# Kernel optimization log

Measured on AMD Instinct MI355X. Metric: run time of the kernel, lower is better.

The kernel has to match this reference:

```python
import jax, jax.numpy as jnp
import numpy as np

EPS = 1e-5
NPOINT = 1024
NSAMPLE = 32


def _bn(x, gamma, beta, axes):
    # batch-norm in training mode (biased variance), channel-last
    m = jnp.mean(x, axes, keepdims=True)
    v = jnp.var(x, axes, keepdims=True)
    return (x - m) * jax.lax.rsqrt(v + EPS) * gamma + beta


def _fps(xyz, npoint):
    # xyz: [B, N, 3] -> indices [B, npoint]; deterministic start at index 0
    xyz = jax.lax.stop_gradient(xyz)
    B, N, _ = xyz.shape

    def step(carry, _):
        dist, far = carry
        c = jnp.take_along_axis(xyz, far[:, None, None], axis=1)  # [B,1,3]
        d = jnp.sum((xyz - c) ** 2, -1)                            # [B,N]
        dist = jnp.minimum(dist, d)
        return (dist, jnp.argmax(dist, -1).astype(jnp.int32)), far

    init = (jnp.full((B, N), 1e10, xyz.dtype), jnp.zeros((B,), jnp.int32))
    _, idx = jax.lax.scan(step, init, None, length=npoint)
    return idx.T  # [B, npoint]


def _sqdist(src, dst):
    # [B,S,C],[B,N,C] -> [B,S,N]
    d = -2.0 * jnp.einsum('bsc,bnc->bsn', src, dst)
    d += jnp.sum(src ** 2, -1)[:, :, None]
    d += jnp.sum(dst ** 2, -1)[:, None, :]
    return d


def _gather(p, idx):
    # p: [B,N,C], idx: [B,...] -> [B,...,C]
    return jax.vmap(lambda a, i: a[i])(p, idx)


def setup_inputs() -> dict:
    key = jax.random.key(0)
    ks = jax.random.split(key, 12)
    B, N, D = 8, 4096, 64
    inp = {
        'xyz': jax.random.normal(ks[0], (B, 3, N), jnp.float32),
        'points': jax.random.normal(ks[1], (B, D, N), jnp.float32),
        # mlp convs (1x1 Conv2d == per-point linear): [out,in]
        'c1_w': jax.random.normal(ks[2], (64, 64), jnp.float32) / 8.0,
        'c1_b': jnp.zeros((64,), jnp.float32),
        'g1': jnp.ones((64,), jnp.float32), 'b1': jnp.zeros((64,), jnp.float32),
        'c2_w': jax.random.normal(ks[3], (128, 64), jnp.float32) / 8.0,
        'c2_b': jnp.zeros((128,), jnp.float32),
        'g2': jnp.ones((128,), jnp.float32), 'b2': jnp.zeros((128,), jnp.float32),
        # weightnet: 3 -> 8 -> 8 -> 16
        'w0_w': jax.random.normal(ks[4], (8, 3), jnp.float32) / np.sqrt(3.0),
        'w0_b': jnp.zeros((8,), jnp.float32),
        'w0_g': jnp.ones((8,), jnp.float32), 'w0_be': jnp.zeros((8,), jnp.float32),
        'w1_w': jax.random.normal(ks[5], (8, 8), jnp.float32) / np.sqrt(8.0),
        'w1_b': jnp.zeros((8,), jnp.float32),
        'w1_g': jnp.ones((8,), jnp.float32), 'w1_be': jnp.zeros((8,), jnp.float32),
        'w2_w': jax.random.normal(ks[6], (16, 8), jnp.float32) / np.sqrt(8.0),
        'w2_b': jnp.zeros((16,), jnp.float32),
        'w2_g': jnp.ones((16,), jnp.float32), 'w2_be': jnp.zeros((16,), jnp.float32),
        # final linear: 16*128 -> 128
        'lin_w': jax.random.normal(ks[7], (128, 16 * 128), jnp.float32) / np.sqrt(2048.0),
        'lin_b': jnp.zeros((128,), jnp.float32),
        'lg': jnp.ones((128,), jnp.float32), 'lb': jnp.zeros((128,), jnp.float32),
    }
    return inp


def reference(xyz, points, c1_w, c1_b, g1, b1, c2_w, c2_b, g2, b2,
              w0_w, w0_b, w0_g, w0_be, w1_w, w1_b, w1_g, w1_be,
              w2_w, w2_b, w2_g, w2_be, lin_w, lin_b, lg, lb):
    B = xyz.shape[0]
    X = jnp.transpose(xyz, (0, 2, 1))      # [B,N,3]
    P = jnp.transpose(points, (0, 2, 1))   # [B,N,D]

    fps_idx = _fps(X, NPOINT)                                      # [B,S]
    new_xyz = jnp.take_along_axis(X, fps_idx[:, :, None], axis=1)  # [B,S,3]

    sqr = _sqdist(jax.lax.stop_gradient(new_xyz), jax.lax.stop_gradient(X))
    _, nidx = jax.lax.top_k(-sqr, NSAMPLE)                         # [B,S,K]

    neigh_xyz = _gather(X, nidx)                                   # [B,S,K,3]
    off = neigh_xyz - new_xyz[:, :, None, :]                       # [B,S,K,3]
    f = _gather(P, nidx)                                           # [B,S,K,D]

    # per-point MLP (1x1 convs + BN2d over (B,K,S) + relu)
    for W, bias, g, be in ((c1_w, c1_b, g1, b1), (c2_w, c2_b, g2, b2)):
        f = jax.nn.relu(_bn(jnp.einsum('bskd,cd->bskc', f, W) + bias, g, be, (0, 1, 2)))

    # WeightNet on offsets
    w = off
    for W, bias, g, be in ((w0_w, w0_b, w0_g, w0_be),
                           (w1_w, w1_b, w1_g, w1_be),
                           (w2_w, w2_b, w2_g, w2_be)):
        w = jax.nn.relu(_bn(jnp.einsum('bskd,cd->bskc', w, W) + bias, g, be, (0, 1, 2)))

    # weighted aggregation over neighbors: [B,S,Cl,16] -> [B,S,Cl*16]
    feats = jnp.einsum('bskc,bskw->bscw', f, w).reshape(B, NPOINT, -1)
    y = feats @ lin_w.T + lin_b                                    # [B,S,128]
    y = jax.nn.relu(_bn(y, lg, lb, (0, 1)))

    return jnp.transpose(new_xyz, (0, 2, 1)), jnp.transpose(y, (0, 2, 1))
```

## Files before the change

kernel.cpp:

```cpp
#include <hip/hip_runtime.h>
#include <hip/hip_bf16.h>

#define BB 8
#define NN 4096
#define DD 64
#define SS 1024
#define KK 32
#define C1 64
#define C2 128

typedef unsigned int uint32;
typedef unsigned long long uint64;

constexpr int BSK = BB * SS * KK;
constexpr int BS  = BB * SS;

#define ST_S1_C1 0
#define ST_S2_C1 64
#define ST_S1_C2 128
#define ST_S2_C2 256
#define ST_S1_W0 384
#define ST_S2_W0 392
#define ST_S1_W1 400
#define ST_S2_W1 408
#define ST_S1_W2 416
#define ST_S2_W2 432
#define ST_S1_Y  448
#define ST_S2_Y  576
#define ST_STRIDE 704
#define N_SLOTS 64

#define PA_A_C1 0
#define PA_C_C1 64
#define PA_A_C2 128
#define PA_C_C2 256
#define PA_A_W0 384
#define PA_C_W0 392
#define PA_A_W1 400
#define PA_C_W1 408
#define PA_A_W2 416
#define PA_C_W2 432
#define PA_A_Y  448
#define PA_C_Y  576

#if __has_builtin(__builtin_amdgcn_update_dpp)
#define HAS_DPP 1
template <int CTRL>
__device__ __forceinline__ double dpp_f64(double x) {
    uint64 u = (uint64)__double_as_longlong(x);
    int lo = (int)(uint32)u, hi = (int)(uint32)(u >> 32);
    int lo2 = __builtin_amdgcn_update_dpp(lo, lo, CTRL, 0xf, 0xf, false);
    int hi2 = __builtin_amdgcn_update_dpp(hi, hi, CTRL, 0xf, 0xf, false);
    return __longlong_as_double((long long)(((uint64)(uint32)hi2 << 32) | (uint32)lo2));
}
__device__ __forceinline__ double wave_max_pack(double k) {
    k = fmax(k, dpp_f64<0x111>(k));
    k = fmax(k, dpp_f64<0x112>(k));
    k = fmax(k, dpp_f64<0x114>(k));
    k = fmax(k, dpp_f64<0x118>(k));
    k = fmax(k, dpp_f64<0x142>(k));
    k = fmax(k, dpp_f64<0x143>(k));
    return k;
}
__device__ __forceinline__ double wave_min_pack(double k) {
    k = fmin(k, dpp_f64<0x111>(k));
    k = fmin(k, dpp_f64<0x112>(k));
    k = fmin(k, dpp_f64<0x114>(k));
    k = fmin(k, dpp_f64<0x118>(k));
    k = fmin(k, dpp_f64<0x142>(k));
    k = fmin(k, dpp_f64<0x143>(k));
    return k;
}
__device__ __forceinline__ uint64 bcast63_u64(double k) {
#if __has_builtin(__builtin_amdgcn_readlane)
    uint64 u = (uint64)__double_as_longlong(k);
    int lo = __builtin_amdgcn_readlane((int)(uint32)u, 63);
    int hi = __builtin_amdgcn_readlane((int)(uint32)(u >> 32), 63);
    return ((uint64)(uint32)hi << 32) | (uint32)lo;
#else
    return (uint64)__double_as_longlong(__shfl(k, 63));
#endif
}
#define FPS_WRITER_LANE 63
template <int CTRL>
__device__ __forceinline__ float dpp_mov_f32(float x) {
    int r = __builtin_amdgcn_update_dpp(__float_as_int(x), __float_as_int(x),
                                        CTRL, 0xf, 0xf, false);
    return __int_as_float(r);
}
__device__ __forceinline__ float wave_sum_f32(float v) {
    v += dpp_mov_f32<0x111>(v);
    v += dpp_mov_f32<0x112>(v);
    v += dpp_mov_f32<0x114>(v);
    v += dpp_mov_f32<0x118>(v);
    v += dpp_mov_f32<0x142>(v);
    v += dpp_mov_f32<0x143>(v);
    return v;
}
#define LIN_WRITER 63
#else
#define HAS_DPP 0
__device__ __forceinline__ double wave_max_pack(double k) {
#pragma unroll
    for (int m = 32; m >= 1; m >>= 1) k = fmax(k, __shfl_xor(k, m));
    return k;
}
__device__ __forceinline__ double wave_min_pack(double k) {
#pragma unroll
    for (int m = 32; m >= 1; m >>= 1) k = fmin(k, __shfl_xor(k, m));
    return k;
}
__device__ __forceinline__ uint64 bcast63_u64(double k) {
    return (uint64)__double_as_longlong(k);
}
#define FPS_WRITER_LANE 0
__device__ __forceinline__ float wave_sum_f32(float v) {
#pragma unroll
    for (int m = 32; m >= 1; m >>= 1) v += __shfl_xor(v, m);
    return v;
}
#define LIN_WRITER 0
#endif

__device__ __forceinline__ uint32 bf16rne(float x) {
    uint32 u = __float_as_uint(x);
    return (u + 0x7fffu + ((u >> 16) & 1u)) >> 16;
}

typedef __attribute__((ext_vector_type(8))) short bf16x8;
typedef __attribute__((ext_vector_type(4))) float f32x4v;

__global__ __launch_bounds__(256) void prep_fps(const float* __restrict__ points,
                                                __hip_bfloat16* __restrict__ ptsT,
                                                const float* __restrict__ c1_w,
                                                const float* __restrict__ c2_w,
                                                const float* __restrict__ lin_w,
                                                float* __restrict__ w1t,
                                                float* __restrict__ w2t,
                                                __hip_bfloat16* __restrict__ linB,
                                                const float* __restrict__ xyz,
                                                float* __restrict__ new_xyz,
                                                float* __restrict__ out0) {
    __shared__ __align__(16) char smu[69696];
    int t = threadIdx.x;
    int blk = blockIdx.x;
    if (blk < 8) {
        float4* xyz4 = (float4*)smu;
        int* hist = (int*)(smu + 65536);
        double* slots = (double*)(smu + 69632);
        int b = blk;
        int wv = t >> 6, lane = t & 63;
        const float* base = xyz + (size_t)b * 3 * NN;
        float px[16], py[16], pz[16], dl[16];
        uint32 lidx[16];
#pragma unroll
        for (int i = 0; i < 16; i++) {
            int n = t + 256 * i;
            px[i] = base[n];
            py[i] = base[NN + n];
            pz[i] = base[2 * NN + n];
            float4 v; v.x = px[i]; v.y = py[i]; v.z = pz[i]; v.w = 0.f;
            xyz4[n] = v;
            dl[i] = 1e10f;
            lidx[i] = (uint32)(NN - 1 - n);
        }
        if (t == 0) hist[0] = 0;
        __syncthreads();
        int far = 0;
        for (int step = 1; step < SS; step++) {
            int p = step & 1;
            float4 c = xyz4[far];
            float cx = c.x, cy = c.y, cz = c.z;
            double k0 = 0.0, k1 = 0.0, k2 = 0.0, k3 = 0.0;
#pragma unroll
            for (int i = 0; i < 16; i++) {
                float dx = __fsub_rn(px[i], cx);
                float dy = __fsub_rn(py[i], cy);
                float dz = __fsub_rn(pz[i], cz);
                float d = __fadd_rn(__fadd_rn(__fmul_rn(dx, dx), __fmul_rn(dy, dy)),
                                    __fmul_rn(dz, dz));
                float nd = fminf(dl[i], d);
                dl[i] = nd;
                uint64 kbits = ((uint64)__float_as_uint(nd) << 32) | lidx[i];
                double kk = __longlong_as_double((long long)kbits);
                if ((i & 3) == 0) k0 = fmax(k0, kk);
                else if ((i & 3) == 1) k1 = fmax(k1, kk);
                else if ((i & 3) == 2) k2 = fmax(k2, kk);
                else k3 = fmax(k3, kk);
            }
            double kbest = fmax(fmax(k0, k1), fmax(k2, k3));
            kbest = wave_max_pack(kbest);
            if (lane == FPS_WRITER_LANE) slots[p * 4 + wv] = kbest;
            __syncthreads();
            double s0 = slots[p * 4 + 0], s1 = slots[p * 4 + 1];
            double s2 = slots[p * 4 + 2], s3 = slots[p * 4 + 3];
            double bk = fmax(fmax(s0, s1), fmax(s2, s3));
            uint64 kb = (uint64)__double_as_longlong(bk);
            int bbx = (NN - 1) - (int)(uint32)(kb & 0xffffffffull);
            far = bbx;
            if (t == 0) hist[step] = bbx;
        }
        __syncthreads();
        for (int s = t; s < SS; s += 256) {
            int idx = hist[s];
            float4 v = xyz4[idx];
            size_t q = (size_t)(b * SS + s);
            new_xyz[q * 3 + 0] = v.x;
            new_xyz[q * 3 + 1] = v.y;
            new_xyz[q * 3 + 2] = v.z;
            out0[(size_t)b * 3 * SS + 0 * SS + s] = v.x;
            out0[(size_t)b * 3 * SS + 1 * SS + s] = v.y;
            out0[(size_t)b * 3 * SS + 2 * SS + s] = v.z;
        }
    } else if (blk < 520) {
        float (*tile)[65] = (float(*)[65])smu;
        int bb = blk - 8;
        int b = bb >> 6;
        int n0 = (bb & 63) * 64;
        for (int i = t; i < 4096; i += 256) {
            int d = i >> 6, n = i & 63;
            tile[d][n] = points[((size_t)b * DD + d) * NN + n0 + n];
        }
        __syncthreads();
        for (int i = t; i < 4096; i += 256) {
            int n = i >> 6, d = i & 63;
            ptsT[((size_t)b * NN + n0 + n) * DD + d] = __float2bfloat16(tile[d][n]);
        }
    } else {
        int i = (blk - 520) * 256 + t;
        if (i < 4096) {
            int d = i >> 6, c = i & 63;
            w1t[d * 64 + c] = c1_w[c * 64 + d];
        }
        int j = i - 4096;
        if (j >= 0 && j < 8192) {
            int d = j >> 7, c = j & 127;
            w2t[d * 128 + c] = c2_w[c * 64 + d];
        }
        int l = i - 12288;
        if (l >= 0 && l < 262144) linB[l] = __float2bfloat16(lin_w[l]);
    }
}

__global__ __launch_bounds__(256) void knn_wave(const float* __restrict__ xyz,
                                                const float* __restrict__ new_xyz,
                                                int* __restrict__ nidx,
                                                float* __restrict__ offs) {
    int wv = threadIdx.x >> 6, lane = threadIdx.x & 63;
    int q = blockIdx.x * 4 + wv;
    int b = q >> 10;
    const float* base = xyz + (size_t)b * 3 * NN;
    float sx = new_xyz[(size_t)q * 3 + 0];
    float sy = new_xyz[(size_t)q * 3 + 1];
    float sz = new_xyz[(size_t)q * 3 + 2];
    float s2 = __fadd_rn(__fadd_rn(__fmul_rn(sx, sx), __fmul_rn(sy, sy)), __fmul_rn(sz, sz));
    float dl[64];
#pragma unroll
    for (int i = 0; i < 64; i++) {
        int n = i * 64 + lane;
        float x = base[n], y = base[NN + n], z = base[2 * NN + n];
        float d2 = __fadd_rn(__fadd_rn(__fmul_rn(x, x), __fmul_rn(y, y)), __fmul_rn(z, z));
        float dot = __fadd_rn(__fadd_rn(__fmul_rn(sx, x), __fmul_rn(sy, y)), __fmul_rn(sz, z));
        float v = __fmul_rn(-2.0f, dot);
        v = __fadd_rn(v, s2);
        v = __fadd_rn(v, d2);
        dl[i] = v;
    }
    const float MASKF = __uint_as_float(0x7F7FFFFFu);
    unsigned long long excl = 0ull;
    for (int k = 0; k < KK; k++) {
        float best = MASKF;
        int bslot = 0;
#pragma unroll
        for (int i = 0; i < 64; i++) {
            bool ok = ((excl >> i) & 1ull) == 0ull;
            float v = ok ? dl[i] : MASKF;
            if (v < best) { best = v; bslot = i; }
        }
        uint64 kbits = ((uint64)__float_as_uint(best) << 32) |
                       (uint32)(bslot * 64 + lane);
        double kb = wave_min_pack(__longlong_as_double((long long)kbits));
        uint64 r = bcast63_u64(kb);
        int bi = (int)(uint32)(r & 0xffffffffull);
        if ((bi & 63) == lane) excl |= (1ull << (bi >> 6));
        if (lane == 0) {
            nidx[(size_t)q * KK + k] = bi;
            size_t oo = ((size_t)q * KK + k) * 3;
            offs[oo + 0] = __fsub_rn(base[bi], sx);
            offs[oo + 1] = __fsub_rn(base[NN + bi], sy);
            offs[oo + 2] = __fsub_rn(base[2 * NN + bi], sz);
        }
    }
}

__device__ __forceinline__ void stage_pts(const __hip_bfloat16* __restrict__ ptsT,
                                          const int* __restrict__ nidx,
                                          int q, int b, int t, float* pts) {
    int k = t >> 3, d8 = t & 7;
    int nn = nidx[(size_t)q * KK + k];
    uint4 u = ((const uint4*)ptsT)[((size_t)b * NN + nn) * 8 + d8];
    float4 lo, hi;
    lo.x = __uint_as_float(u.x << 16); lo.y = __uint_as_float(u.x & 0xffff0000u);
    lo.z = __uint_as_float(u.y << 16); lo.w = __uint_as_float(u.y & 0xffff0000u);
    hi.x = __uint_as_float(u.z << 16); hi.y = __uint_as_float(u.z & 0xffff0000u);
    hi.z = __uint_as_float(u.w << 16); hi.w = __uint_as_float(u.w & 0xffff0000u);
    *(float4*)&pts[k * 64 + d8 * 8] = lo;
    *(float4*)&pts[k * 64 + d8 * 8 + 4] = hi;
}

__global__ __launch_bounds__(256) void pass_a(const __hip_bfloat16* __restrict__ ptsT,
                                              const int* __restrict__ nidx,
                                              const float* __restrict__ offs,
                                              const float* __restrict__ w1t,
                                              const float* __restrict__ c1_b,
                                              const float* __restrict__ w0_w,
                                              const float* __restrict__ w0_b,
                                              float* __restrict__ stats,
                                              float* __restrict__ f1pre,
                                              int emit_f1) {
    __shared__ __align__(16) float pts[2048];
    __shared__ float red1[256], red2[256];
    int blk = blockIdx.x, t = threadIdx.x;
    int b = blk >> 10;
    int slot = blk & (N_SLOTS - 1);
    stage_pts(ptsT, nidx, blk, b, t, pts);
    __syncthreads();
    int c = t & 63, kg = t >> 6;
    float bias = c1_b[c];
    float acc[8];
#pragma unroll
    for (int j = 0; j < 8; j++) acc[j] = bias;
    for (int d4 = 0; d4 < 16; d4++) {
        float w0 = w1t[(4 * d4 + 0) * 64 + c];
        float w1v = w1t[(4 * d4 + 1) * 64 + c];
        float w2v = w1t[(4 * d4 + 2) * 64 + c];
        float w3 = w1t[(4 * d4 + 3) * 64 + c];
#pragma unroll
        for (int j = 0; j < 8; j++) {
            const float4 p = *(const float4*)&pts[(kg + 4 * j) * 64 + 4 * d4];
            acc[j] = fmaf(p.x, w0, acc[j]);
            acc[j] = fmaf(p.y, w1v, acc[j]);
            acc[j] = fmaf(p.z, w2v, acc[j]);
            acc[j] = fmaf(p.w, w3, acc[j]);
        }
    }
    if (emit_f1) {
#pragma unroll
        for (int j = 0; j < 8; j++)
            f1pre[(size_t)blk * 2048 + j * 256 + t] = acc[j];
    }
    float s1 = 0.f, s2 = 0.f;
#pragma unroll
    for (int j = 0; j < 8; j++) { s1 += acc[j]; s2 += acc[j] * acc[j]; }
    red1[t] = s1;
    red2[t] = s2;
    __syncthreads();
    if (t < 64) {
        atomicAdd(&stats[slot * ST_STRIDE + ST_S1_C1 + t],
                  red1[t] + red1[t + 64] + red1[t + 128] + red1[t + 192]);
        atomicAdd(&stats[slot * ST_STRIDE + ST_S2_C1 + t],
                  red2[t] + red2[t + 64] + red2[t + 128] + red2[t + 192]);
    }
    int k0 = t >> 3, c0 = t & 7;
    size_t oo = ((size_t)blk * KK + k0) * 3;
    float h = w0_b[c0];
    h = fmaf(offs[oo + 0], w0_w[c0 * 3 + 0], h);
    h = fmaf(offs[oo + 1], w0_w[c0 * 3 + 1], h);
    h = fmaf(offs[oo + 2], w0_w[c0 * 3 + 2], h);
    __syncthreads();
    red1[t] = h;
    red2[t] = h * h;
    __syncthreads();
    if (t < 8) {
        float a = 0.f, q = 0.f;
        for (int j = t; j < 256; j += 8) { a += red1[j]; q += red2[j]; }
        atomicAdd(&stats[slot * ST_STRIDE + ST_S1_W0 + t], a);
        atomicAdd(&stats[slot * ST_STRIDE + ST_S2_W0 + t], q);
    }
}

__device__ __forceinline__ void fin_one(const float* stats, float* params,
                                        const float* g, const float* be,
                                        int s1o, int s2o, int ao, int co,
                                        int nch, float inv, int t) {
    if (t < nch) {
        float s1 = 0.f, s2 = 0.f;
        for (int s = 0; s < N_SLOTS; s++) {
            s1 += stats[s * ST_STRIDE + s1o + t];
            s2 += stats[s * ST_STRIDE + s2o + t];
        }
        float m = s1 * inv;
        float v = s2 * inv - m * m;
        float a = g[t] * rsqrtf(v + 1e-5f);
        params[ao + t] = a;
        params[co + t] = be[t] - m * a;
    }
}

__global__ void finalize_bn(const float* __restrict__ stats, float* __restrict__ params,
                            const float* __restrict__ g, const float* __restrict__ be,
                            int s1o, int s2o, int ao, int co, int nch, float inv) {
    fin_one(stats, params, g, be, s1o, s2o, ao, co, nch, inv, threadIdx.x);
}

__global__ void finalize_two(const float* __restrict__ stats, float* __restrict__ params,
                             const float* __restrict__ gA, const float* __restrict__ beA,
                             int s1A, int s2A, int aA, int cA, int nA, float invA,
                             const float* __restrict__ gB, const float* __restrict__ beB,
                             int s1B, int s2B, int aB, int cB, int nB, float invB) {
    if (blockIdx.x == 0)
        fin_one(stats, params, gA, beA, s1A, s2A, aA, cA, nA, invA, threadIdx.x);
    else
        fin_one(stats, params, gB, beB, s1B, s2B, aB, cB, nB, invB, threadIdx.x);
}

__global__ __launch_bounds__(256) void pass_b(const __hip_bfloat16* __restrict__ ptsT,
                                              const int* __restrict__ nidx,
                                              const float* __restrict__ offs,
                                              const float* __restrict__ w1t,
                                              const float* __restrict__ c1_b,
                                              const float* __restrict__ w2t,
                                              const float* __restrict__ c2_b,
                                              const float* __restrict__ w0_w,
                                              const float* __restrict__ w0_b,
                                              const float* __restrict__ w1_w,
                                              const float* __restrict__ w1_b,
                                              const float* __restrict__ params,
                                              float* __restrict__ stats) {
    __shared__ __align__(16) float pts[2048];
    __shared__ __align__(16) float f1[2048];
    __shared__ float red1[256], red2[256];
    int blk = blockIdx.x, t = threadIdx.x;
    int b = blk >> 10;
    int slot = blk & (N_SLOTS - 1);
    stage_pts(ptsT, nidx, blk, b, t, pts);
    __syncthreads();
    {
        int c = t & 63, kg = t >> 6;
        float a1 = params[PA_A_C1 + c], cc1 = params[PA_C_C1 + c], bias = c1_b[c];
        float acc[8];
#pragma unroll
        for (int j = 0; j < 8; j++) acc[j] = bias;
        for (int d4 = 0; d4 < 16; d4++) {
// ... 239 lines not shown
#pragma unroll
        for (int q = 0; q < 8; q++) h = fmaf(h1[q], w2_w[cw * 8 + q], h);
        wg[idx] = fmaxf(fmaf(h, params[PA_A_W2 + cw], params[PA_C_W2 + cw]), 0.f);
    }
}

__global__ __launch_bounds__(256) void tail_nl2(const float* __restrict__ f2pre,
                                                const float* __restrict__ offs,
                                                const float* __restrict__ w0_w,
                                                const float* __restrict__ w0_b,
                                                const float* __restrict__ w1_w,
                                                const float* __restrict__ w1_b,
                                                const float* __restrict__ w2_w,
                                                const float* __restrict__ w2_b,
                                                const float* __restrict__ params,
                                                float* __restrict__ featsF) {
    __shared__ __align__(16) float sm[6656];
    float* f2    = sm;
    float* wg    = sm + 4096;
    float* feats = sm + 4608;
    int blk = blockIdx.x, t = threadIdx.x;
    weightnet_to_lds(offs, w0_w, w0_b, w1_w, w1_b, w2_w, w2_b, params, blk, t, wg);
    {
        int c = t & 127;
        float a2 = params[PA_A_C2 + c], cc2 = params[PA_C_C2 + c];
#pragma unroll
        for (int i = 0; i < 16; i++) {
            float v = f2pre[(size_t)blk * 4096 + i * 256 + t];
            f2[i * 256 + t] = fmaxf(fmaf(v, a2, cc2), 0.f);
        }
    }
    __syncthreads();
    {
        int cc = t & 127, wh = t >> 7;
        float acc[8];
#pragma unroll
        for (int i = 0; i < 8; i++) acc[i] = 0.f;
        for (int k = 0; k < KK; k++) {
            float fv = f2[k * 128 + cc];
            const float4 wa = *(const float4*)&wg[k * 16 + 8 * wh];
            const float4 wb = *(const float4*)&wg[k * 16 + 8 * wh + 4];
            acc[0] = fmaf(fv, wa.x, acc[0]);
            acc[1] = fmaf(fv, wa.y, acc[1]);
            acc[2] = fmaf(fv, wa.z, acc[2]);
            acc[3] = fmaf(fv, wa.w, acc[3]);
            acc[4] = fmaf(fv, wb.x, acc[4]);
            acc[5] = fmaf(fv, wb.y, acc[5]);
            acc[6] = fmaf(fv, wb.z, acc[6]);
            acc[7] = fmaf(fv, wb.w, acc[7]);
        }
        *(float4*)&feats[cc * 16 + 8 * wh]     = *(float4*)&acc[0];
        *(float4*)&feats[cc * 16 + 8 * wh + 4] = *(float4*)&acc[4];
    }
    __syncthreads();
#pragma unroll
    for (int i = 0; i < 8; i++)
        featsF[(size_t)blk * 2048 + i * 256 + t] = feats[i * 256 + t];
}

__global__ __launch_bounds__(256) void fused_tail_nl(
        const __hip_bfloat16* __restrict__ ptsT, const int* __restrict__ nidx,
        const float* __restrict__ offs,
        const float* __restrict__ w1t, const float* __restrict__ c1_b,
        const float* __restrict__ w2t, const float* __restrict__ c2_b,
        const float* __restrict__ w0_w, const float* __restrict__ w0_b,
        const float* __restrict__ w1_w, const float* __restrict__ w1_b,
        const float* __restrict__ w2_w, const float* __restrict__ w2_b,
        const float* __restrict__ params, float* __restrict__ featsF) {
    __shared__ __align__(16) float sm[8704];
    float* pts   = sm;
    float* f1    = sm + 2048;
    float* f2    = sm + 4096;
    float* wg    = sm + 8192;
    int blk = blockIdx.x, t = threadIdx.x;
    int b = blk >> 10;
    stage_pts(ptsT, nidx, blk, b, t, pts);
    weightnet_to_lds(offs, w0_w, w0_b, w1_w, w1_b, w2_w, w2_b, params, blk, t, wg);
    __syncthreads();
    {
        int c = t & 63, kg = t >> 6;
        float a1 = params[PA_A_C1 + c], cc1 = params[PA_C_C1 + c], bias = c1_b[c];
        float acc[8];
#pragma unroll
        for (int j = 0; j < 8; j++) acc[j] = bias;
        for (int d4 = 0; d4 < 16; d4++) {
            float w0 = w1t[(4 * d4 + 0) * 64 + c];
            float w1v = w1t[(4 * d4 + 1) * 64 + c];
            float w2v = w1t[(4 * d4 + 2) * 64 + c];
            float w3 = w1t[(4 * d4 + 3) * 64 + c];
#pragma unroll
            for (int j = 0; j < 8; j++) {
                const float4 p = *(const float4*)&pts[(kg + 4 * j) * 64 + 4 * d4];
                acc[j] = fmaf(p.x, w0, acc[j]);
                acc[j] = fmaf(p.y, w1v, acc[j]);
                acc[j] = fmaf(p.z, w2v, acc[j]);
                acc[j] = fmaf(p.w, w3, acc[j]);
            }
        }
#pragma unroll
        for (int j = 0; j < 8; j++)
            f1[(kg + 4 * j) * 64 + c] = fmaxf(fmaf(acc[j], a1, cc1), 0.f);
    }
    __syncthreads();
    {
        int c = t & 127, kg = t >> 7;
        float a2 = params[PA_A_C2 + c], cc2 = params[PA_C_C2 + c], bias = c2_b[c];
        float acc[16];
#pragma unroll
        for (int j = 0; j < 16; j++) acc[j] = bias;
        for (int d4 = 0; d4 < 16; d4++) {
            float w0 = w2t[(4 * d4 + 0) * 128 + c];
            float w1v = w2t[(4 * d4 + 1) * 128 + c];
            float w2v = w2t[(4 * d4 + 2) * 128 + c];
            float w3 = w2t[(4 * d4 + 3) * 128 + c];
#pragma unroll
            for (int j = 0; j < 16; j++) {
                const float4 p = *(const float4*)&f1[(kg + 2 * j) * 64 + 4 * d4];
                acc[j] = fmaf(p.x, w0, acc[j]);
                acc[j] = fmaf(p.y, w1v, acc[j]);
                acc[j] = fmaf(p.z, w2v, acc[j]);
                acc[j] = fmaf(p.w, w3, acc[j]);
            }
        }
#pragma unroll
        for (int j = 0; j < 16; j++)
            f2[(kg + 2 * j) * 128 + c] = fmaxf(fmaf(acc[j], a2, cc2), 0.f);
    }
    __syncthreads();
    {
        int cc = t & 127, wh = t >> 7;
        float acc[8];
#pragma unroll
        for (int i = 0; i < 8; i++) acc[i] = 0.f;
        for (int k = 0; k < KK; k++) {
            float fv = f2[k * 128 + cc];
            const float4 wa = *(const float4*)&wg[k * 16 + 8 * wh];
            const float4 wb = *(const float4*)&wg[k * 16 + 8 * wh + 4];
            acc[0] = fmaf(fv, wa.x, acc[0]);
            acc[1] = fmaf(fv, wa.y, acc[1]);
            acc[2] = fmaf(fv, wa.z, acc[2]);
            acc[3] = fmaf(fv, wa.w, acc[3]);
            acc[4] = fmaf(fv, wb.x, acc[4]);
            acc[5] = fmaf(fv, wb.y, acc[5]);
            acc[6] = fmaf(fv, wb.z, acc[6]);
            acc[7] = fmaf(fv, wb.w, acc[7]);
        }
        *(float4*)&pts[cc * 16 + 8 * wh]     = *(float4*)&acc[0];
        *(float4*)&pts[cc * 16 + 8 * wh + 4] = *(float4*)&acc[4];
    }
    __syncthreads();
#pragma unroll
    for (int i = 0; i < 8; i++)
        featsF[(size_t)blk * 2048 + i * 256 + t] = sm[i * 256 + t];
}

__global__ __launch_bounds__(256) void fused_tail(
        const __hip_bfloat16* __restrict__ ptsT, const int* __restrict__ nidx,
        const float* __restrict__ offs,
        const float* __restrict__ w1t, const float* __restrict__ c1_b,
        const float* __restrict__ w2t, const float* __restrict__ c2_b,
        const float* __restrict__ w0_w, const float* __restrict__ w0_b,
        const float* __restrict__ w1_w, const float* __restrict__ w1_b,
        const float* __restrict__ w2_w, const float* __restrict__ w2_b,
        const __hip_bfloat16* __restrict__ linB, const float* __restrict__ lin_b,
        const float* __restrict__ params, float* __restrict__ stats,
        float* __restrict__ ypre) {
    __shared__ __align__(16) float sm[8704];
    float* pts   = sm;
    float* f1    = sm + 2048;
    float* f2    = sm + 4096;
    float* wg    = sm + 8192;
    int blk = blockIdx.x, t = threadIdx.x;
    int b = blk >> 10;
    int slot = blk & (N_SLOTS - 1);
    stage_pts(ptsT, nidx, blk, b, t, pts);
    weightnet_to_lds(offs, w0_w, w0_b, w1_w, w1_b, w2_w, w2_b, params, blk, t, wg);
    __syncthreads();
    {
        int c = t & 63, kg = t >> 6;
        float a1 = params[PA_A_C1 + c], cc1 = params[PA_C_C1 + c], bias = c1_b[c];
        float acc[8];
#pragma unroll
        for (int j = 0; j < 8; j++) acc[j] = bias;
        for (int d4 = 0; d4 < 16; d4++) {
            float w0 = w1t[(4 * d4 + 0) * 64 + c];
            float w1v = w1t[(4 * d4 + 1) * 64 + c];
            float w2v = w1t[(4 * d4 + 2) * 64 + c];
            float w3 = w1t[(4 * d4 + 3) * 64 + c];
#pragma unroll
            for (int j = 0; j < 8; j++) {
                const float4 p = *(const float4*)&pts[(kg + 4 * j) * 64 + 4 * d4];
                acc[j] = fmaf(p.x, w0, acc[j]);
                acc[j] = fmaf(p.y, w1v, acc[j]);
                acc[j] = fmaf(p.z, w2v, acc[j]);
                acc[j] = fmaf(p.w, w3, acc[j]);
            }
        }
#pragma unroll
        for (int j = 0; j < 8; j++)
            f1[(kg + 4 * j) * 64 + c] = fmaxf(fmaf(acc[j], a1, cc1), 0.f);
    }
    __syncthreads();
    {
        int c = t & 127, kg = t >> 7;
        float a2 = params[PA_A_C2 + c], cc2 = params[PA_C_C2 + c], bias = c2_b[c];
        float acc[16];
#pragma unroll
        for (int j = 0; j < 16; j++) acc[j] = bias;
        for (int d4 = 0; d4 < 16; d4++) {
            float w0 = w2t[(4 * d4 + 0) * 128 + c];
            float w1v = w2t[(4 * d4 + 1) * 128 + c];
            float w2v = w2t[(4 * d4 + 2) * 128 + c];
            float w3 = w2t[(4 * d4 + 3) * 128 + c];
#pragma unroll
            for (int j = 0; j < 16; j++) {
                const float4 p = *(const float4*)&f1[(kg + 2 * j) * 64 + 4 * d4];
                acc[j] = fmaf(p.x, w0, acc[j]);
                acc[j] = fmaf(p.y, w1v, acc[j]);
                acc[j] = fmaf(p.z, w2v, acc[j]);
                acc[j] = fmaf(p.w, w3, acc[j]);
            }
        }
#pragma unroll
        for (int j = 0; j < 16; j++)
            f2[(kg + 2 * j) * 128 + c] = fmaxf(fmaf(acc[j], a2, cc2), 0.f);
    }
    __syncthreads();
    {
        int cc = t & 127, wh = t >> 7;
        float acc[8];
#pragma unroll
        for (int i = 0; i < 8; i++) acc[i] = 0.f;
        for (int k = 0; k < KK; k++) {
            float fv = f2[k * 128 + cc];
            const float4 wa = *(const float4*)&wg[k * 16 + 8 * wh];
            const float4 wb = *(const float4*)&wg[k * 16 + 8 * wh + 4];
            acc[0] = fmaf(fv, wa.x, acc[0]);
            acc[1] = fmaf(fv, wa.y, acc[1]);
            acc[2] = fmaf(fv, wa.z, acc[2]);
            acc[3] = fmaf(fv, wa.w, acc[3]);
            acc[4] = fmaf(fv, wb.x, acc[4]);
            acc[5] = fmaf(fv, wb.y, acc[5]);
            acc[6] = fmaf(fv, wb.z, acc[6]);
            acc[7] = fmaf(fv, wb.w, acc[7]);
        }
        *(float4*)&pts[cc * 16 + 8 * wh]     = *(float4*)&acc[0];
        *(float4*)&pts[cc * 16 + 8 * wh + 4] = *(float4*)&acc[4];
    }
    __syncthreads();
    float* feats = pts;
    {
        int wv = t >> 6, lane = t & 63;
        float4 fv[8];
#pragma unroll
        for (int j0 = 0; j0 < 8; j0++)
            fv[j0] = *(const float4*)&feats[(j0 * 64 + lane) * 4];
        for (int oi = 0; oi < 32; oi++) {
            int o = wv * 32 + oi;
            const uint2* lw = (const uint2*)(linB + (size_t)o * 2048);
            float acc = 0.f;
#pragma unroll
            for (int j0 = 0; j0 < 8; j0++) {
                uint2 u = lw[j0 * 64 + lane];
                acc = fmaf(fv[j0].x, __uint_as_float(u.x << 16), acc);
                acc = fmaf(fv[j0].y, __uint_as_float(u.x & 0xffff0000u), acc);
                acc = fmaf(fv[j0].z, __uint_as_float(u.y << 16), acc);
                acc = fmaf(fv[j0].w, __uint_as_float(u.y & 0xffff0000u), acc);
            }
            acc = wave_sum_f32(acc);
            if (lane == LIN_WRITER) {
                float y = acc + lin_b[o];
                ypre[(size_t)blk * 128 + o] = y;
                atomicAdd(&stats[slot * ST_STRIDE + ST_S1_Y + o], y);
                atomicAdd(&stats[slot * ST_STRIDE + ST_S2_Y + o], y * y);
            }
        }
    }
}

__global__ __launch_bounds__(256) void linear_mm16(const float* __restrict__ featsF,
                                                   const __hip_bfloat16* __restrict__ linB,
                                                   const float* __restrict__ lin_b,
                                                   float* __restrict__ stats,
                                                   float* __restrict__ ypre) {
    __shared__ __align__(16) unsigned short Ah[2][16 * 72];
    __shared__ __align__(16) unsigned short Al[2][16 * 72];
    __shared__ __align__(16) unsigned short Bsm[2][128 * 72];
    int t = threadIdx.x;
    int q0 = blockIdx.x * 16;
    int slot = blockIdx.x & (N_SLOTS - 1);
    int qa = t >> 4, pa = t & 15;
    int ob = t >> 1, pb = t & 1;
    int lane = t & 63, w = t >> 6;
    int lg = lane >> 4, ln = lane & 15;
    int qb_base = q0 + lg * 4;

    f32x4v acc0 = {0.f, 0.f, 0.f, 0.f};
    f32x4v acc1 = {0.f, 0.f, 0.f, 0.f};

    const uint4* gA0 = (const uint4*)(featsF + (size_t)(q0 + qa) * 2048);
    const uint4* gB0 = (const uint4*)(linB + (size_t)ob * 2048);

    uint4 ra, rb0, rb1, rb2, rb3;
    ra  = gA0[pa];
    rb0 = gB0[pb * 4 + 0];
    rb1 = gB0[pb * 4 + 1];
    rb2 = gB0[pb * 4 + 2];
    rb3 = gB0[pb * 4 + 3];

    for (int kc = 0; kc < 32; kc++) {
        int buf = kc & 1;
        {
            float f0 = __uint_as_float(ra.x), f1v = __uint_as_float(ra.y);
            float f2v = __uint_as_float(ra.z), f3 = __uint_as_float(ra.w);
            uint32 h0 = bf16rne(f0), h1 = bf16rne(f1v), h2 = bf16rne(f2v), h3 = bf16rne(f3);
            uint2 hv;
            hv.x = h0 | (h1 << 16); hv.y = h2 | (h3 << 16);
            *(uint2*)&Ah[buf][qa * 72 + pa * 4] = hv;
            uint32 l0 = bf16rne(f0 - __uint_as_float(h0 << 16));
            uint32 l1 = bf16rne(f1v - __uint_as_float(h1 << 16));
            uint32 l2 = bf16rne(f2v - __uint_as_float(h2 << 16));
            uint32 l3 = bf16rne(f3 - __uint_as_float(h3 << 16));
            uint2 lv;
            lv.x = l0 | (l1 << 16); lv.y = l2 | (l3 << 16);
            *(uint2*)&Al[buf][qa * 72 + pa * 4] = lv;
            *(uint4*)&Bsm[buf][ob * 72 + pb * 32 + 0]  = rb0;
            *(uint4*)&Bsm[buf][ob * 72 + pb * 32 + 8]  = rb1;
            *(uint4*)&Bsm[buf][ob * 72 + pb * 32 + 16] = rb2;
            *(uint4*)&Bsm[buf][ob * 72 + pb * 32 + 24] = rb3;
        }
        __syncthreads();
        if (kc + 1 < 32) {
            ra  = gA0[(kc + 1) * 16 + pa];
            rb0 = gB0[(kc + 1) * 8 + pb * 4 + 0];
            rb1 = gB0[(kc + 1) * 8 + pb * 4 + 1];
            rb2 = gB0[(kc + 1) * 8 + pb * 4 + 2];
            rb3 = gB0[(kc + 1) * 8 + pb * 4 + 3];
        }
#pragma unroll
        for (int s = 0; s < 2; s++) {
            int ko = s * 32 + lg * 8;
            bf16x8 ah = *(const bf16x8*)&Ah[buf][ln * 72 + ko];
            bf16x8 al = *(const bf16x8*)&Al[buf][ln * 72 + ko];
            bf16x8 b0 = *(const bf16x8*)&Bsm[buf][(w * 32 + 0  + ln) * 72 + ko];
            bf16x8 b1 = *(const bf16x8*)&Bsm[buf][(w * 32 + 16 + ln) * 72 + ko];
            acc0 = __builtin_amdgcn_mfma_f32_16x16x32_bf16(ah, b0, acc0, 0, 0, 0);
            acc0 = __builtin_amdgcn_mfma_f32_16x16x32_bf16(al, b0, acc0, 0, 0, 0);
            acc1 = __builtin_amdgcn_mfma_f32_16x16x32_bf16(ah, b1, acc1, 0, 0, 0);
            acc1 = __builtin_amdgcn_mfma_f32_16x16x32_bf16(al, b1, acc1, 0, 0, 0);
        }
    }
    {
        int o0 = w * 32 + 0  + ln;
        int o1 = w * 32 + 16 + ln;
        float lb0 = lin_b[o0], lb1 = lin_b[o1];
        float s1a = 0.f, s2a = 0.f, s1b = 0.f, s2b = 0.f;
#pragma unroll
        for (int r = 0; r < 4; r++) {
            size_t qrow = (size_t)(qb_base + r) * 128;
            float y0 = acc0[r] + lb0;
            float y1 = acc1[r] + lb1;
            ypre[qrow + o0] = y0;
            ypre[qrow + o1] = y1;
            s1a += y0; s2a += y0 * y0;
            s1b += y1; s2b += y1 * y1;
        }
        atomicAdd(&stats[slot * ST_STRIDE + ST_S1_Y + o0], s1a);
        atomicAdd(&stats[slot * ST_STRIDE + ST_S2_Y + o0], s2a);
        atomicAdd(&stats[slot * ST_STRIDE + ST_S1_Y + o1], s1b);
        atomicAdd(&stats[slot * ST_STRIDE + ST_S2_Y + o1], s2b);
    }
}

__global__ __launch_bounds__(256) void bn_y(const float* __restrict__ ypre,
                                            const float* __restrict__ stats,
                                            const float* __restrict__ lg,
                                            const float* __restrict__ lb,
                                            float* __restrict__ out1) {
    __shared__ float tile[64 * 133];
    __shared__ float pa[128], pc[128];
    int blk = blockIdx.x;
    int b = blk >> 4;
    int s0 = (blk & 15) * 64;
    int t = threadIdx.x;
    if (t < 128) {
        float s1 = 0.f, s2 = 0.f;
        for (int s = 0; s < N_SLOTS; s++) {
            s1 += stats[s * ST_STRIDE + ST_S1_Y + t];
            s2 += stats[s * ST_STRIDE + ST_S2_Y + t];
        }
        const float inv = 1.f / (float)BS;
        float m = s1 * inv;
        float v = s2 * inv - m * m;
        float a = lg[t] * rsqrtf(v + 1e-5f);
        pa[t] = a;
        pc[t] = lb[t] - m * a;
    }
#pragma unroll
    for (int i = 0; i < 32; i++) {
        int idx = i * 256 + t;
        int s = idx >> 7, c = idx & 127;
        tile[s * 133 + c] = ypre[(((size_t)b << 10) + s0 + s) * 128 + c];
    }
    __syncthreads();
#pragma unroll
    for (int i = 0; i < 32; i++) {
        int idx = i * 256 + t;
        int c = idx >> 6, s = idx & 63;
        float v = tile[s * 133 + c];
        out1[((size_t)b * 128 + c) * 1024 + s0 + s] =
            fmaxf(fmaf(v, pa[c], pc[c]), 0.f);
    }
}

extern "C" void kernel_launch(void* const* d_in, const int* in_sizes, int n_in,
                              void* d_out, int out_size, void* d_ws, size_t ws_size,
                              hipStream_t stream) {
    const float* xyz    = (const float*)d_in[0];
    const float* points = (const float*)d_in[1];
    const float* c1_w = (const float*)d_in[2];
    const float* c1_b = (const float*)d_in[3];
    const float* g1   = (const float*)d_in[4];
    const float* b1   = (const float*)d_in[5];
    const float* c2_w = (const float*)d_in[6];
    const float* c2_b = (const float*)d_in[7];
    const float* g2   = (const float*)d_in[8];
    const float* b2   = (const float*)d_in[9];
    const float* w0_w = (const float*)d_in[10];
    const float* w0_b = (const float*)d_in[11];
    const float* w0_g = (const float*)d_in[12];
    const float* w0_be= (const float*)d_in[13];
    const float* w1_w = (const float*)d_in[14];
    const float* w1_b = (const float*)d_in[15];
    const float* w1_g = (const float*)d_in[16];
    const float* w1_be= (const float*)d_in[17];
    const float* w2_w = (const float*)d_in[18];
    const float* w2_b = (const float*)d_in[19];
    const float* w2_g = (const float*)d_in[20];
    const float* w2_be= (const float*)d_in[21];
    const float* lin_w= (const float*)d_in[22];
    const float* lin_b= (const float*)d_in[23];
    const float* lg   = (const float*)d_in[24];
    const float* lb   = (const float*)d_in[25];

    float* out0 = (float*)d_out;
    float* out1 = out0 + (size_t)BB * 3 * SS;

    char* wsb = (char*)d_ws;
    int*   nidx    = (int*)(wsb + 0);
    float* offs    = (float*)(wsb + 1048576);
    float* new_xyz = (float*)(wsb + 4194304);
    float* ypre    = (float*)(wsb + 4292608);
    __hip_bfloat16* ptsT = (__hip_bfloat16*)(wsb + 8486912);
    float* w1t     = (float*)(wsb + 12681216);
    float* w2t     = (float*)(wsb + 12697600);
    __hip_bfloat16* linB = (__hip_bfloat16*)(wsb + 12730368);
    float* stats   = (float*)(wsb + 13254656);
    float* params  = (float*)(wsb + 13434880);
    float* featsF  = (float*)(wsb + 13437696);
    float* f1pre   = featsF;
    float* f2pre   = (float*)(wsb + 80546560);

    const size_t NEED1 = 13437696ull + 67108864ull;
    const size_t NEED2 = 80546560ull + 134217728ull;
    const int tier = (ws_size >= NEED2) ? 2 : (ws_size >= NEED1) ? 1 : 0;

    hipMemsetAsync(stats, 0, N_SLOTS * ST_STRIDE * sizeof(float), stream);

    prep_fps<<<1592, 256, 0, stream>>>(points, ptsT, c1_w, c2_w, lin_w, w1t, w2t,
                                       linB, xyz, new_xyz, out0);
    knn_wave<<<BS / 4, 256, 0, stream>>>(xyz, new_xyz, nidx, offs);

    pass_a<<<BS, 256, 0, stream>>>(ptsT, nidx, offs, w1t, c1_b, w0_w, w0_b, stats,
                                   f1pre, tier == 2 ? 1 : 0);
    finalize_two<<<2, 128, 0, stream>>>(stats, params,
                                        g1, b1, ST_S1_C1, ST_S2_C1, PA_A_C1, PA_C_C1, 64, 1.f / BSK,
                                        w0_g, w0_be, ST_S1_W0, ST_S2_W0, PA_A_W0, PA_C_W0, 8, 1.f / BSK);

    if (tier == 2) {
        pass_b2<<<BS, 256, 0, stream>>>(f1pre, offs, w2t, c2_b,
                                        w0_w, w0_b, w1_w, w1_b, params, stats, f2pre);
    } else {
        pass_b<<<BS, 256, 0, stream>>>(ptsT, nidx, offs, w1t, c1_b, w2t, c2_b,
                                       w0_w, w0_b, w1_w, w1_b, params, stats);
    }
    finalize_two<<<2, 128, 0, stream>>>(stats, params,
                                        g2, b2, ST_S1_C2, ST_S2_C2, PA_A_C2, PA_C_C2, 128, 1.f / BSK,
                                        w1_g, w1_be, ST_S1_W1, ST_S2_W1, PA_A_W1, PA_C_W1, 8, 1.f / BSK);

    pass_w2<<<BSK / 256, 256, 0, stream>>>(offs, w0_w, w0_b, w1_w, w1_b, w2_w, w2_b,
                                           params, stats);
    finalize_bn<<<1, 128, 0, stream>>>(stats, params, w2_g, w2_be,
                                       ST_S1_W2, ST_S2_W2, PA_A_W2, PA_C_W2, 16, 1.f / BSK);

    if (tier == 2) {
        tail_nl2<<<BS, 256, 0, stream>>>(f2pre, offs, w0_w, w0_b, w1_w, w1_b,
                                         w2_w, w2_b, params, featsF);
        linear_mm16<<<BS / 16, 256, 0, stream>>>(featsF, linB, lin_b, stats, ypre);
    } else if (tier == 1) {
        fused_tail_nl<<<BS, 256, 0, stream>>>(ptsT, nidx, offs, w1t, c1_b, w2t, c2_b,
                                              w0_w, w0_b, w1_w, w1_b, w2_w, w2_b,
                                              params, featsF);
        linear_mm16<<<BS / 16, 256, 0, stream>>>(featsF, linB, lin_b, stats, ypre);
    } else {
        fused_tail<<<BS, 256, 0, stream>>>(ptsT, nidx, offs, w1t, c1_b, w2t, c2_b,
                                           w0_w, w0_b, w1_w, w1_b, w2_w, w2_b,
                                           linB, lin_b, params, stats, ypre);
    }

    bn_y<<<BB * 16, 256, 0, stream>>>(ypre, stats, lg, lb, out1);
}
```

Baseline: 1.113 ms.

## Fuse FPS and kNN into one kernel with progress-flag streaming

Merges the FPS/prep kernel and the kNN kernel into a single launch. FPS blocks publish new_xyz in chunks of 32 sampled points and advance a per-batch progress counter with release atomics, while kNN blocks spin with acquire loads until the centroids they need exist. kNN work then overlaps the long serial FPS loop instead of waiting for it to finish. This risks deadlock if kNN blocks occupy all CUs before the FPS blocks are scheduled, adds spin-wait overhead, and removes the tier-0 fused_tail fallback.

Result: no change. 1.109 ms (-0.3%).

```diff
diff --git a/kernel.cpp b/kernel.cpp
--- a/kernel.cpp
+++ b/kernel.cpp
@@ -40,8 +40,6 @@
 #define PA_C_W1 408
 #define PA_A_W2 416
 #define PA_C_W2 432
-#define PA_A_Y  448
-#define PA_C_Y  576
 
 #if __has_builtin(__builtin_amdgcn_update_dpp)
 #define HAS_DPP 1
@@ -130,17 +128,20 @@
 typedef __attribute__((ext_vector_type(8))) short bf16x8;
 typedef __attribute__((ext_vector_type(4))) float f32x4v;
 
-__global__ __launch_bounds__(256) void prep_fps(const float* __restrict__ points,
-                                                __hip_bfloat16* __restrict__ ptsT,
-                                                const float* __restrict__ c1_w,
-                                                const float* __restrict__ c2_w,
-                                                const float* __restrict__ lin_w,
-                                                float* __restrict__ w1t,
-                                                float* __restrict__ w2t,
-                                                __hip_bfloat16* __restrict__ linB,
-                                                const float* __restrict__ xyz,
-                                                float* __restrict__ new_xyz,
-                                                float* __restrict__ out0) {
+__global__ __launch_bounds__(256) void prep_fps_knn(const float* __restrict__ points,
+                                                    __hip_bfloat16* __restrict__ ptsT,
+                                                    const float* __restrict__ c1_w,
+                                                    const float* __restrict__ c2_w,
+                                                    const float* __restrict__ lin_w,
+                                                    float* __restrict__ w1t,
+                                                    float* __restrict__ w2t,
+                                                    __hip_bfloat16* __restrict__ linB,
+                                                    const float* __restrict__ xyz,
+                                                    float* __restrict__ new_xyz,
+                                                    float* __restrict__ out0,
+                                                    int* __restrict__ progress,
+                                                    int* __restrict__ nidx,
+                                                    float* __restrict__ offs) {
     __shared__ __align__(16) char smu[69696];
     int t = threadIdx.x;
     int blk = blockIdx.x;
@@ -199,6 +200,20 @@
             int bbx = (NN - 1) - (int)(uint32)(kb & 0xffffffffull);
             far = bbx;
             if (t == 0) hist[step] = bbx;
+            if ((step & 31) == 1 && step > 32) {
+                if (t < 32) {
+                    int s2p = step - 33 + t;
+                    int idx2 = hist[s2p];
+                    float4 v2 = xyz4[idx2];
+                    size_t qq = (size_t)(b * SS + s2p) * 3;
+                    new_xyz[qq + 0] = v2.x;
+                    new_xyz[qq + 1] = v2.y;
+                    new_xyz[qq + 2] = v2.z;
+                }
+                if (t == 0)
+                    __hip_atomic_store(&progress[b], step - 1, __ATOMIC_RELEASE,
+                                       __HIP_MEMORY_SCOPE_AGENT);
+            }
         }
         __syncthreads();
         for (int s = t; s < SS; s += 256) {
@@ -212,6 +227,11 @@
             out0[(size_t)b * 3 * SS + 1 * SS + s] = v.y;
             out0[(size_t)b * 3 * SS + 2 * SS + s] = v.z;
         }
+        __threadfence();
+        __syncthreads();
+        if (t == 0)
+            __hip_atomic_store(&progress[b], SS, __ATOMIC_RELEASE,
+                               __HIP_MEMORY_SCOPE_AGENT);
     } else if (blk < 520) {
         float (*tile)[65] = (float(*)[65])smu;
         int bb = blk - 8;
@@ -226,7 +246,7 @@
             int n = i >> 6, d = i & 63;
             ptsT[((size_t)b * NN + n0 + n) * DD + d] = __float2bfloat16(tile[d][n]);
         }
-    } else {
+    } else if (blk < 1592) {
         int i = (blk - 520) * 256 + t;
         if (i < 4096) {
             int d = i >> 6, c = i & 63;
@@ -239,56 +259,57 @@
         }
         int l = i - 12288;
         if (l >= 0 && l < 262144) linB[l] = __float2bfloat16(lin_w[l]);
-    }
-}
-
-__global__ __launch_bounds__(256) void knn_wave(const float* __restrict__ xyz,
-                                                const float* __restrict__ new_xyz,
-                                                int* __restrict__ nidx,
-                                                float* __restrict__ offs) {
-    int wv = threadIdx.x >> 6, lane = threadIdx.x & 63;
-    int q = blockIdx.x * 4 + wv;
-    int b = q >> 10;
-    const float* base = xyz + (size_t)b * 3 * NN;
-    float sx = new_xyz[(size_t)q * 3 + 0];
-    float sy = new_xyz[(size_t)q * 3 + 1];
-    float sz = new_xyz[(size_t)q * 3 + 2];
-    float s2 = __fadd_rn(__fadd_rn(__fmul_rn(sx, sx), __fmul_rn(sy, sy)), __fmul_rn(sz, sz));
-    float dl[64];
-#pragma unroll
-    for (int i = 0; i < 64; i++) {
-        int n = i * 64 + lane;
-        float x = base[n], y = base[NN + n], z = base[2 * NN + n];
-        float d2 = __fadd_rn(__fadd_rn(__fmul_rn(x, x), __fmul_rn(y, y)), __fmul_rn(z, z));
-        float dot = __fadd_rn(__fadd_rn(__fmul_rn(sx, x), __fmul_rn(sy, y)), __fmul_rn(sz, z));
-        float v = __fmul_rn(-2.0f, dot);
-        v = __fadd_rn(v, s2);
-        v = __fadd_rn(v, d2);
-        dl[i] = v;
-    }
-    const float MASKF = __uint_as_float(0x7F7FFFFFu);
-    unsigned long long excl = 0ull;
-    for (int k = 0; k < KK; k++) {
-        float best = MASKF;
-        int bslot = 0;
+    } else {
+        int cb = blk - 1592;
+        int wv = t >> 6, lane = t & 63;
+        int bq = cb & 7;
+        int pos = ((cb >> 3) << 2) + wv;
+        int q = bq * SS + pos;
+        int needed = pos + 1;
+        while (__hip_atomic_load(&progress[bq], __ATOMIC_ACQUIRE,
+                                 __HIP_MEMORY_SCOPE_AGENT) < needed)
+            __builtin_amdgcn_s_sleep(8);
+        const float* base = xyz + (size_t)bq * 3 * NN;
+        float sx = new_xyz[(size_t)q * 3 + 0];
+        float sy = new_xyz[(size_t)q * 3 + 1];
+        float sz = new_xyz[(size_t)q * 3 + 2];
+        float s2 = __fadd_rn(__fadd_rn(__fmul_rn(sx, sx), __fmul_rn(sy, sy)), __fmul_rn(sz, sz));
+        float dl[64];
 #pragma unroll
         for (int i = 0; i < 64; i++) {
-            bool ok = ((excl >> i) & 1ull) == 0ull;
-            float v = ok ? dl[i] : MASKF;
-            if (v < best) { best = v; bslot = i; }
-        }
-        uint64 kbits = ((uint64)__float_as_uint(best) << 32) |
-                       (uint32)(bslot * 64 + lane);
-        double kb = wave_min_pack(__longlong_as_double((long long)kbits));
-        uint64 r = bcast63_u64(kb);
-        int bi = (int)(uint32)(r & 0xffffffffull);
-        if ((bi & 63) == lane) excl |= (1ull << (bi >> 6));
-        if (lane == 0) {
-            nidx[(size_t)q * KK + k] = bi;
-            size_t oo = ((size_t)q * KK + k) * 3;
-            offs[oo + 0] = __fsub_rn(base[bi], sx);
-            offs[oo + 1] = __fsub_rn(base[NN + bi], sy);
-            offs[oo + 2] = __fsub_rn(base[2 * NN + bi], sz);
+            int n = i * 64 + lane;
+            float x = base[n], y = base[NN + n], z = base[2 * NN + n];
+            float d2 = __fadd_rn(__fadd_rn(__fmul_rn(x, x), __fmul_rn(y, y)), __fmul_rn(z, z));
+            float dot = __fadd_rn(__fadd_rn(__fmul_rn(sx, x), __fmul_rn(sy, y)), __fmul_rn(sz, z));
+            float v = __fmul_rn(-2.0f, dot);
+            v = __fadd_rn(v, s2);
+            v = __fadd_rn(v, d2);
+            dl[i] = v;
+        }
+        const float MASKF = __uint_as_float(0x7F7FFFFFu);
+        unsigned long long excl = 0ull;
+        for (int k = 0; k < KK; k++) {
+            float best = MASKF;
+            int bslot = 0;
+#pragma unroll
+            for (int i = 0; i < 64; i++) {
+                bool ok = ((excl >> i) & 1ull) == 0ull;
+                float v = ok ? dl[i] : MASKF;
+                if (v < best) { best = v; bslot = i; }
+            }
+            uint64 kbits = ((uint64)__float_as_uint(best) << 32) |
+                           (uint32)(bslot * 64 + lane);
+            double kb = wave_min_pack(__longlong_as_double((long long)kbits));
+            uint64 r = bcast63_u64(kb);
+            int bi = (int)(uint32)(r & 0xffffffffull);
+            if ((bi & 63) == lane) excl |= (1ull << (bi >> 6));
+            if (lane == 0) {
+                nidx[(size_t)q * KK + k] = bi;
+                size_t oo = ((size_t)q * KK + k) * 3;
+                offs[oo + 0] = __fsub_rn(base[bi], sx);
+                offs[oo + 1] = __fsub_rn(base[NN + bi], sy);
+                offs[oo + 2] = __fsub_rn(base[2 * NN + bi], sz);
+            }
         }
     }
 }
@@ -834,130 +855,6 @@
 #pragma unroll
     for (int i = 0; i < 8; i++)
         featsF[(size_t)blk * 2048 + i * 256 + t] = sm[i * 256 + t];
-}
-
-__global__ __launch_bounds__(256) void fused_tail(
-        const __hip_bfloat16* __restrict__ ptsT, const int* __restrict__ nidx,
-        const float* __restrict__ offs,
-        const float* __restrict__ w1t, const float* __restrict__ c1_b,
-        const float* __restrict__ w2t, const float* __restrict__ c2_b,
-        const float* __restrict__ w0_w, const float* __restrict__ w0_b,
-        const float* __restrict__ w1_w, const float* __restrict__ w1_b,
-        const float* __restrict__ w2_w, const float* __restrict__ w2_b,
-        const __hip_bfloat16* __restrict__ linB, const float* __restrict__ lin_b,
-        const float* __restrict__ params, float* __restrict__ stats,
-        float* __restrict__ ypre) {
-    __shared__ __align__(16) float sm[8704];
-    float* pts   = sm;
-    float* f1    = sm + 2048;
-    float* f2    = sm + 4096;
-    float* wg    = sm + 8192;
-    int blk = blockIdx.x, t = threadIdx.x;
-    int b = blk >> 10;
-    int slot = blk & (N_SLOTS - 1);
-    stage_pts(ptsT, nidx, blk, b, t, pts);
-    weightnet_to_lds(offs, w0_w, w0_b, w1_w, w1_b, w2_w, w2_b, params, blk, t, wg);
-    __syncthreads();
-    {
-        int c = t & 63, kg = t >> 6;
-        float a1 = params[PA_A_C1 + c], cc1 = params[PA_C_C1 + c], bias = c1_b[c];
-        float acc[8];
-#pragma unroll
-        for (int j = 0; j < 8; j++) acc[j] = bias;
-        for (int d4 = 0; d4 < 16; d4++) {
-            float w0 = w1t[(4 * d4 + 0) * 64 + c];
-            float w1v = w1t[(4 * d4 + 1) * 64 + c];
-            float w2v = w1t[(4 * d4 + 2) * 64 + c];
-            float w3 = w1t[(4 * d4 + 3) * 64 + c];
-#pragma unroll
-            for (int j = 0; j < 8; j++) {
-                const float4 p = *(const float4*)&pts[(kg + 4 * j) * 64 + 4 * d4];
-                acc[j] = fmaf(p.x, w0, acc[j]);
-                acc[j] = fmaf(p.y, w1v, acc[j]);
-                acc[j] = fmaf(p.z, w2v, acc[j]);
-                acc[j] = fmaf(p.w, w3, acc[j]);
-            }
-        }
-#pragma unroll
-        for (int j = 0; j < 8; j++)
-            f1[(kg + 4 * j) * 64 + c] = fmaxf(fmaf(acc[j], a1, cc1), 0.f);
-    }
-    __syncthreads();
-    {
-        int c = t & 127, kg = t >> 7;
-        float a2 = params[PA_A_C2 + c], cc2 = params[PA_C_C2 + c], bias = c2_b[c];
-        float acc[16];
-#pragma unroll
-        for (int j = 0; j < 16; j++) acc[j] = bias;
-        for (int d4 = 0; d4 < 16; d4++) {
-            float w0 = w2t[(4 * d4 + 0) * 128 + c];
-            float w1v = w2t[(4 * d4 + 1) * 128 + c];
-            float w2v = w2t[(4 * d4 + 2) * 128 + c];
-            float w3 = w2t[(4 * d4 + 3) * 128 + c];
-#pragma unroll
-            for (int j = 0; j < 16; j++) {
-                const float4 p = *(const float4*)&f1[(kg + 2 * j) * 64 + 4 * d4];
-                acc[j] = fmaf(p.x, w0, acc[j]);
-                acc[j] = fmaf(p.y, w1v, acc[j]);
-                acc[j] = fmaf(p.z, w2v, acc[j]);
-                acc[j] = fmaf(p.w, w3, acc[j]);
-            }
-        }
-#pragma unroll
-        for (int j = 0; j < 16; j++)
-            f2[(kg + 2 * j) * 128 + c] = fmaxf(fmaf(acc[j], a2, cc2), 0.f);
-    }
-    __syncthreads();
-    {
-        int cc = t & 127, wh = t >> 7;
-        float acc[8];
-#pragma unroll
-        for (int i = 0; i < 8; i++) acc[i] = 0.f;
-        for (int k = 0; k < KK; k++) {
-            float fv = f2[k * 128 + cc];
-            const float4 wa = *(const float4*)&wg[k * 16 + 8 * wh];
-            const float4 wb = *(const float4*)&wg[k * 16 + 8 * wh + 4];
-            acc[0] = fmaf(fv, wa.x, acc[0]);
-            acc[1] = fmaf(fv, wa.y, acc[1]);
-            acc[2] = fmaf(fv, wa.z, acc[2]);
-            acc[3] = fmaf(fv, wa.w, acc[3]);
-            acc[4] = fmaf(fv, wb.x, acc[4]);
-            acc[5] = fmaf(fv, wb.y, acc[5]);
-            acc[6] = fmaf(fv, wb.z, acc[6]);
-            acc[7] = fmaf(fv, wb.w, acc[7]);
-        }
-        *(float4*)&pts[cc * 16 + 8 * wh]     = *(float4*)&acc[0];
-        *(float4*)&pts[cc * 16 + 8 * wh + 4] = *(float4*)&acc[4];
-    }
-    __syncthreads();
-    float* feats = pts;
-    {
-        int wv = t >> 6, lane = t & 63;
-        float4 fv[8];
-#pragma unroll
-        for (int j0 = 0; j0 < 8; j0++)
-            fv[j0] = *(const float4*)&feats[(j0 * 64 + lane) * 4];
-        for (int oi = 0; oi < 32; oi++) {
-            int o = wv * 32 + oi;
-            const uint2* lw = (const uint2*)(linB + (size_t)o * 2048);
-            float acc = 0.f;
-#pragma unroll
-            for (int j0 = 0; j0 < 8; j0++) {
-                uint2 u = lw[j0 * 64 + lane];
-                acc = fmaf(fv[j0].x, __uint_as_float(u.x << 16), acc);
-                acc = fmaf(fv[j0].y, __uint_as_float(u.x & 0xffff0000u), acc);
-                acc = fmaf(fv[j0].z, __uint_as_float(u.y << 16), acc);
-                acc = fmaf(fv[j0].w, __uint_as_float(u.y & 0xffff0000u), acc);
-            }
-            acc = wave_sum_f32(acc);
-            if (lane == LIN_WRITER) {
-                float y = acc + lin_b[o];
-                ypre[(size_t)blk * 128 + o] = y;
-                atomicAdd(&stats[slot * ST_STRIDE + ST_S1_Y + o], y);
-                atomicAdd(&stats[slot * ST_STRIDE + ST_S2_Y + o], y * y);
-            }
-        }
-    }
 }
 
 __global__ __launch_bounds__(256) void linear_mm16(const float* __restrict__ featsF,
@@ -1139,6 +1036,7 @@
     __hip_bfloat16* linB = (__hip_bfloat16*)(wsb + 12730368);
     float* stats   = (float*)(wsb + 13254656);
     float* params  = (float*)(wsb + 13434880);
+    int*   progress= (int*)(wsb + 13436672);
     float* featsF  = (float*)(wsb + 13437696);
     float* f1pre   = featsF;
     float* f2pre   = (float*)(wsb + 80546560);
@@ -1148,10 +1046,11 @@
     const int tier = (ws_size >= NEED2) ? 2 : (ws_size >= NEED1) ? 1 : 0;
 
     hipMemsetAsync(stats, 0, N_SLOTS * ST_STRIDE * sizeof(float), stream);
-
-    prep_fps<<<1592, 256, 0, stream>>>(points, ptsT, c1_w, c2_w, lin_w, w1t, w2t,
-                                       linB, xyz, new_xyz, out0);
-    knn_wave<<<BS / 4, 256, 0, stream>>>(xyz, new_xyz, nidx, offs);
+    hipMemsetAsync(progress, 0, 64, stream);
+
+    prep_fps_knn<<<3640, 256, 0, stream>>>(points, ptsT, c1_w, c2_w, lin_w, w1t, w2t,
+                                           linB, xyz, new_xyz, out0,
+                                           progress, nidx, offs);
 
     pass_a<<<BS, 256, 0, stream>>>(ptsT, nidx, offs, w1t, c1_b, w0_w, w0_b, stats,
                                    f1pre, tier == 2 ? 1 : 0);
@@ -1179,15 +1078,11 @@
         tail_nl2<<<BS, 256, 0, stream>>>(f2pre, offs, w0_w, w0_b, w1_w, w1_b,
                                          w2_w, w2_b, params, featsF);
         linear_mm16<<<BS / 16, 256, 0, stream>>>(featsF, linB, lin_b, stats, ypre);
-    } else if (tier == 1) {
+    } else {
         fused_tail_nl<<<BS, 256, 0, stream>>>(ptsT, nidx, offs, w1t, c1_b, w2t, c2_b,
                                               w0_w, w0_b, w1_w, w1_b, w2_w, w2_b,
                                               params, featsF);
         linear_mm16<<<BS / 16, 256, 0, stream>>>(featsF, linB, lin_b, stats, ypre);
-    } else {
-        fused_tail<<<BS, 256, 0, stream>>>(ptsT, nidx, offs, w1t, c1_b, w2t, c2_b,
-                                           w0_w, w0_b, w1_w, w1_b, w2_w, w2_b,
-                                           linB, lin_b, params, stats, ypre);
     }
 
     bn_y<<<BB * 16, 256, 0, stream>>>(ypre, stats, lg, lb, out1);
```
